# Optimization experiments

Hardware: AMD Instinct MI355X
Metric: run time of the kernel (lower is better)

Reference implementation:

```python
import jax, jax.numpy as jnp
import numpy as np

N_NODES = 100000
IN_DIM = 128
OUT_DIM = 128


def setup_inputs() -> dict:
    key = jax.random.key(0)
    ks = jax.random.split(key, 10)
    # entry counts must be multiples of the edge arity (shape)
    e1, e2, e3 = 300000, 600000, 600000  # arities 1, 2, 3 -> 300k/300k/200k hyperedges
    return {
        "x": jax.random.normal(ks[0], (N_NODES, IN_DIM), dtype=jnp.float32),
        "edge_idx_r1": jax.random.randint(ks[1], (2, e1), 0, N_NODES, dtype=jnp.int32),
        "edge_idx_r2": jax.random.randint(ks[2], (2, e2), 0, N_NODES, dtype=jnp.int32),
        "edge_idx_r3": jax.random.randint(ks[3], (2, e3), 0, N_NODES, dtype=jnp.int32),
        "A_r1": jax.random.normal(ks[4], (IN_DIM * 1, OUT_DIM), dtype=jnp.float32) * np.sqrt(2.0 / (IN_DIM * 1 + OUT_DIM)),
        "A_r2": jax.random.normal(ks[5], (IN_DIM * 2, OUT_DIM), dtype=jnp.float32) * np.sqrt(2.0 / (IN_DIM * 2 + OUT_DIM)),
        "A_r3": jax.random.normal(ks[6], (IN_DIM * 3, OUT_DIM), dtype=jnp.float32) * np.sqrt(2.0 / (IN_DIM * 3 + OUT_DIM)),
        "C_w": jax.random.normal(ks[7], (OUT_DIM, IN_DIM), dtype=jnp.float32) * (1.0 / np.sqrt(IN_DIM)),
        "C_b": jax.random.normal(ks[8], (OUT_DIM,), dtype=jnp.float32) * 0.01,
    }


def _edge_type_messages(x, edge_idx, A, arity, n_nodes):
    # edge_idx: [2, groups*arity]; row0 = src node ids, row1 reshaped -> dest = col 0
    dest = edge_idx[1].reshape(-1, arity)[:, 0]              # [groups]
    src = x[edge_idx[0]].reshape(-1, x.shape[1] * arity)     # [groups, in_dim*arity]
    msg = src @ A                                            # [groups, out_dim]
    # degree normalization within this edge type (== 1/counts from torch.unique)
    counts = jnp.zeros((n_nodes,), dtype=msg.dtype).at[dest].add(1.0)
    msg = msg * (1.0 / counts[dest])[:, None]
    return dest, msg


def reference(x, edge_idx_r1, edge_idx_r2, edge_idx_r3, A_r1, A_r2, A_r3, C_w, C_b):
    n = x.shape[0]
    agg = jnp.zeros((n, C_w.shape[0]), dtype=x.dtype)
    for ei, A, arity in ((edge_idx_r1, A_r1, 1), (edge_idx_r2, A_r2, 2), (edge_idx_r3, A_r3, 3)):
        dest, msg = _edge_type_messages(x, ei, A, arity, n)
        agg = agg.at[dest].add(msg)
    return x @ C_w.T + C_b + agg
```

## Files before the change

### kernel.cpp

```cpp
#include <hip/hip_runtime.h>

#define N_NODES 100000
#define DIM 128

typedef __attribute__((ext_vector_type(8))) short bf16x8;
typedef __attribute__((ext_vector_type(4))) float f32x4;
typedef __attribute__((ext_vector_type(8))) unsigned short ushort8;

__device__ __forceinline__ unsigned short f2bf(float f) {
    union { float f; unsigned u; } v; v.f = f;
    unsigned u = v.u + 0x7FFFu + ((v.u >> 16) & 1u);
    return (unsigned short)(u >> 16);
}
__device__ __forceinline__ float bl(unsigned u) { return __uint_as_float(u << 16); }
__device__ __forceinline__ float bh(unsigned u) { return __uint_as_float(u & 0xFFFF0000u); }

__device__ __forceinline__ void gload_lds16(const void* g, void* l) {
    __builtin_amdgcn_global_load_lds((const __attribute__((address_space(1))) void*)g,
                                     (__attribute__((address_space(3))) void*)l, 16, 0, 0);
}

__device__ __forceinline__ void acc2(float4& a, uint2 v) {
    a.x += bl(v.x); a.y += bh(v.x); a.z += bl(v.y); a.w += bh(v.y);
}
__device__ __forceinline__ void red4(float4& a) {
    a.x += __shfl_xor(a.x, 32); a.y += __shfl_xor(a.y, 32);
    a.z += __shfl_xor(a.z, 32); a.w += __shfl_xor(a.w, 32);
}
__device__ __forceinline__ uint2 pack4s(float4 a, float inv) {
    uint2 r;
    r.x = (unsigned)f2bf(a.x * inv) | ((unsigned)f2bf(a.y * inv) << 16);
    r.y = (unsigned)f2bf(a.z * inv) | ((unsigned)f2bf(a.w * inv) << 16);
    return r;
}

__global__ void prep_kernel(const float* __restrict__ x, unsigned short* __restrict__ xb,
                            int n8, const int* __restrict__ e1d,
                            const int* __restrict__ e2d, const int* __restrict__ e3d,
                            int ng1, int ng12, int ngall, int* __restrict__ counts,
                            const float* __restrict__ A1, const float* __restrict__ A2,
                            const float* __restrict__ A3, const float* __restrict__ Cw,
                            unsigned short* __restrict__ bts, int nxblocks) {
    if ((int)blockIdx.x < nxblocks) {
        int i = blockIdx.x * 256 + threadIdx.x;
        if (i < n8) {
            const float4* p = reinterpret_cast<const float4*>(x) + (size_t)i * 2;
            float4 a = p[0], b = p[1];
            ushort8 o;
            o[0] = f2bf(a.x); o[1] = f2bf(a.y); o[2] = f2bf(a.z); o[3] = f2bf(a.w);
            o[4] = f2bf(b.x); o[5] = f2bf(b.y); o[6] = f2bf(b.z); o[7] = f2bf(b.w);
            *reinterpret_cast<ushort8*>(xb + (size_t)i * 8) = o;
        }
        if (i < ng1) atomicAdd(&counts[e1d[i]], 1);
        else if (i < ng12) atomicAdd(&counts[N_NODES + e2d[(size_t)(i - ng1) * 2]], 1);
        else if (i < ngall) atomicAdd(&counts[2 * N_NODES + e3d[(size_t)(i - ng12) * 3]], 1);
    } else {
        int kg = (blockIdx.x - nxblocks) * 2 + (threadIdx.x >> 7);
        int c = threadIdx.x & 127;
        float v;
        int slice, kp;
        if (kg < 128)      { slice = 0; kp = kg; v = A1[(size_t)kg * 128 + c]; }
        else if (kg < 384) { int k = kg - 128; slice = 1 + (k >> 7); kp = k & 127; v = A2[(size_t)k * 128 + c]; }
        else if (kg < 768) { int k = kg - 384; slice = 3 + (k >> 7); kp = k & 127; v = A3[(size_t)k * 128 + c]; }
        else               { int k = kg - 768; slice = 6; kp = k; v = Cw[(size_t)c * 128 + k]; }
        bts[(size_t)slice * 16384 + c * 128 + kp] = f2bf(v);
    }
}

__global__ __launch_bounds__(256) void scan_p1(const int* __restrict__ counts,
                                               int* __restrict__ partials) {
    __shared__ int red[256];
    int type = blockIdx.y, blk = blockIdx.x, tid = threadIdx.x;
    int base = blk * 4096 + tid * 16;
    int s = 0;
#pragma unroll
    for (int j = 0; j < 16; ++j) {
        int i = base + j;
        s += (i < N_NODES) ? counts[(size_t)type * N_NODES + i] : 0;
    }
    red[tid] = s;
    __syncthreads();
    for (int off = 128; off > 0; off >>= 1) {
        if (tid < off) red[tid] += red[tid + off];
        __syncthreads();
    }
    if (tid == 0) partials[type * 32 + blk] = red[0];
}

__global__ __launch_bounds__(256) void scan_p3(const int* __restrict__ counts,
                                               const int* __restrict__ partials,
                                               int* __restrict__ cursor) {
    __shared__ int tsum[256];
    __shared__ int baseoff;
    int type = blockIdx.y, blk = blockIdx.x, tid = threadIdx.x;
    if (tid == 0) {
        int r = 0;
        for (int b = 0; b < blk; ++b) r += partials[type * 32 + b];
        baseoff = r;
    }
    int base = blk * 4096 + tid * 16;
    int v[16];
    int s = 0;
#pragma unroll
    for (int j = 0; j < 16; ++j) {
        int i = base + j;
        v[j] = (i < N_NODES) ? counts[(size_t)type * N_NODES + i] : 0;
        s += v[j];
    }
    tsum[tid] = s;
    __syncthreads();
    for (int off = 1; off < 256; off <<= 1) {
        int t2 = (tid >= off) ? tsum[tid - off] : 0;
        __syncthreads();
        tsum[tid] += t2;
        __syncthreads();
    }
    int run = tsum[tid] - s + baseoff;
#pragma unroll
    for (int j = 0; j < 16; ++j) {
        int i = base + j;
        if (i < N_NODES) cursor[(size_t)type * N_NODES + i] = run;
        run += v[j];
    }
}

__global__ void scatter_all_kernel(const int* __restrict__ e1, const int* __restrict__ e2,
                                   const int* __restrict__ e3, int ne1, int ne2, int ne3,
                                   int ng1, int ng12, int ngall, int* __restrict__ cursor,
                                   int* __restrict__ s1, int2* __restrict__ s2,
                                   int4* __restrict__ s3) {
    int g = blockIdx.x * 256 + threadIdx.x;
    if (g < ng1) {
        int d = e1[ne1 + g];
        s1[atomicAdd(&cursor[d], 1)] = e1[g] << 8;
    } else if (g < ng12) {
        int k = g - ng1;
        int d = e2[ne2 + 2 * (size_t)k];
        int2 v; v.x = e2[2 * (size_t)k] << 8; v.y = e2[2 * (size_t)k + 1] << 8;
        s2[atomicAdd(&cursor[N_NODES + d], 1)] = v;
    } else if (g < ngall) {
        int k = g - ng12;
        int d = e3[ne3 + 3 * (size_t)k];
        int4 v; v.x = e3[3 * (size_t)k] << 8; v.y = e3[3 * (size_t)k + 1] << 8;
        v.z = e3[3 * (size_t)k + 2] << 8; v.w = 0;
        s3[atomicAdd(&cursor[2 * N_NODES + d], 1)] = v;
    }
}

__global__ __launch_bounds__(256) void aggregate_x_kernel(
    const unsigned short* __restrict__ xb,
    const int* __restrict__ s1, const int2* __restrict__ s2, const int4* __restrict__ s3,
    const int* __restrict__ counts, const int* __restrict__ ends,
    unsigned short* __restrict__ gbf)
{
    int d = blockIdx.x * 4 + (threadIdx.x >> 6);
    if (d >= N_NODES) return;
    const int l = threadIdx.x & 63, hw = l >> 5, sl = l & 31;
    const char* xp = (const char*)xb + sl * 8;
    float4 a0 = {0,0,0,0}, a1 = {0,0,0,0}, a2 = {0,0,0,0};
    float4 a3 = {0,0,0,0}, a4 = {0,0,0,0}, a5 = {0,0,0,0};

    const int c1 = counts[d], c2 = counts[N_NODES + d], c3 = counts[2 * N_NODES + d];
    const int E1 = ends[d], E2 = ends[N_NODES + d], E3 = ends[2 * N_NODES + d];

    {
        int i = E1 - c1 + hw;
        for (; i + 2 < E1; i += 4) {
            int o0 = s1[i], o1 = s1[i + 2];
            uint2 v0 = *reinterpret_cast<const uint2*>(xp + o0);
            uint2 v1 = *reinterpret_cast<const uint2*>(xp + o1);
            acc2(a0, v0); acc2(a0, v1);
        }
        if (i < E1) acc2(a0, *reinterpret_cast<const uint2*>(xp + s1[i]));
    }
    {
        int i = E2 - c2 + hw;
        for (; i + 2 < E2; i += 4) {
            int2 p0 = s2[i], p1 = s2[i + 2];
            uint2 va0 = *reinterpret_cast<const uint2*>(xp + p0.x);
            uint2 vb0 = *reinterpret_cast<const uint2*>(xp + p0.y);
            uint2 va1 = *reinterpret_cast<const uint2*>(xp + p1.x);
            uint2 vb1 = *reinterpret_cast<const uint2*>(xp + p1.y);
            acc2(a1, va0); acc2(a2, vb0); acc2(a1, va1); acc2(a2, vb1);
        }
        if (i < E2) {
            int2 p = s2[i];
            acc2(a1, *reinterpret_cast<const uint2*>(xp + p.x));
            acc2(a2, *reinterpret_cast<const uint2*>(xp + p.y));
        }
    }
    {
        int i = E3 - c3 + hw;
        for (; i + 2 < E3; i += 4) {
            int4 p0 = s3[i], p1 = s3[i + 2];
            uint2 va0 = *reinterpret_cast<const uint2*>(xp + p0.x);
            uint2 vb0 = *reinterpret_cast<const uint2*>(xp + p0.y);
            uint2 vc0 = *reinterpret_cast<const uint2*>(xp + p0.z);
            uint2 va1 = *reinterpret_cast<const uint2*>(xp + p1.x);
            uint2 vb1 = *reinterpret_cast<const uint2*>(xp + p1.y);
            uint2 vc1 = *reinterpret_cast<const uint2*>(xp + p1.z);
            acc2(a3, va0); acc2(a4, vb0); acc2(a5, vc0);
            acc2(a3, va1); acc2(a4, vb1); acc2(a5, vc1);
        }
        if (i < E3) {
            int4 p = s3[i];
            acc2(a3, *reinterpret_cast<const uint2*>(xp + p.x));
            acc2(a4, *reinterpret_cast<const uint2*>(xp + p.y));
            acc2(a5, *reinterpret_cast<const uint2*>(xp + p.z));
        }
    }
    red4(a0); red4(a1); red4(a2); red4(a3); red4(a4); red4(a5);
    if (hw == 0) {
        const float i1 = c1 ? 1.f / (float)c1 : 0.f;
        const float i2 = c2 ? 1.f / (float)c2 : 0.f;
        const float i3 = c3 ? 1.f / (float)c3 : 0.f;
        *reinterpret_cast<uint2*>(gbf + ((size_t)0 * N_NODES + d) * 128 + sl * 4) = pack4s(a0, i1);
        *reinterpret_cast<uint2*>(gbf + ((size_t)1 * N_NODES + d) * 128 + sl * 4) = pack4s(a1, i2);
        *reinterpret_cast<uint2*>(gbf + ((size_t)2 * N_NODES + d) * 128 + sl * 4) = pack4s(a2, i2);
        *reinterpret_cast<uint2*>(gbf + ((size_t)3 * N_NODES + d) * 128 + sl * 4) = pack4s(a3, i3);
        *reinterpret_cast<uint2*>(gbf + ((size_t)4 * N_NODES + d) * 128 + sl * 4) = pack4s(a4, i3);
        *reinterpret_cast<uint2*>(gbf + ((size_t)5 * N_NODES + d) * 128 + sl * 4) = pack4s(a5, i3);
    }
}

__global__ __launch_bounds__(256, 2) void gemm_out_kernel(
    const unsigned short* __restrict__ xb, const unsigned short* __restrict__ gbf,
    const unsigned short* __restrict__ bts, const float* __restrict__ Cb,
    float* __restrict__ out, int nnodes)
{
    __shared__ __align__(16) char smem[65536];

    const int tid = threadIdx.x;
    const int w = tid >> 6, l = tid & 63;
    const int g0 = blockIdx.x * 128;
    const int lrow = l & 15, lk = l >> 4;
    const int wr = (w & 1) * 64, wc = (w >> 1) * 64;

    const int q = (((l & 7) ^ (l >> 3)) << 4);
    const int inner = q & 63;
    const int rpq = ((l >> 3) << 1) + (q >> 6);

    int aoff[4];
#pragma unroll
    for (int mi = 0; mi < 4; ++mi) {
        int r = wr + mi * 16 + lrow;
        int P = r >> 1;
        aoff[mi] = P * 128 + ((((r & 1) << 6) | (lk << 4)) ^ ((P & 7) << 4));
    }

    f32x4 acc[4][4];
#pragma unroll
    for (int mi = 0; mi < 4; ++mi)
#pragma unroll
        for (int ni = 0; ni < 4; ++ni) acc[mi][ni] = (f32x4){0.f, 0.f, 0.f, 0.f};

    auto STAGE = [&](int c, int buf) {
#pragma unroll
        for (int i = 0; i < 2; ++i) {
            int u = w * 2 + i;
            int r = u * 16 + rpq;
            int row = (g0 + r < nnodes) ? g0 + r : 0;
            const char* src = (c < 6)
                ? (const char*)gbf + ((size_t)c * N_NODES + row) * 256
                : (const char*)xb + (size_t)row * 256;
#pragma unroll
            for (int t2 = 0; t2 < 4; ++t2)
                gload_lds16(src + t2 * 64 + inner, smem + buf * 32768 + t2 * 8192 + u * 1024);
        }
    };

    STAGE(0, 0);
    asm volatile("s_waitcnt vmcnt(0)" ::: "memory");
    __builtin_amdgcn_s_barrier();
    asm volatile("" ::: "memory");

    for (int c = 0; c < 7; ++c) {
        if (c + 1 < 7) STAGE(c + 1, (c + 1) & 1);
        const int bb = (c & 1) * 32768;
        bf16x8 bgall[4][4];
#pragma unroll
        for (int ks = 0; ks < 4; ++ks)
#pragma unroll
            for (int ni = 0; ni < 4; ++ni)
                bgall[ks][ni] = *reinterpret_cast<const bf16x8*>(
                    bts + (size_t)c * 16384 + (wc + ni * 16 + lrow) * 128 + ks * 32 + lk * 8);
#pragma unroll
        for (int ks = 0; ks < 4; ++ks) {
            bf16x8 af[4];
#pragma unroll
            for (int mi = 0; mi < 4; ++mi)
                af[mi] = *reinterpret_cast<const bf16x8*>(smem + bb + ks * 8192 + aoff[mi]);
            __builtin_amdgcn_s_setprio(1);
#pragma unroll
            for (int mi = 0; mi < 4; ++mi)
#pragma unroll
                for (int ni = 0; ni < 4; ++ni)
                    acc[mi][ni] = __builtin_amdgcn_mfma_f32_16x16x32_bf16(
                        af[mi], bgall[ks][ni], acc[mi][ni], 0, 0, 0);
            __builtin_amdgcn_s_setprio(0);
        }
        asm volatile("s_waitcnt vmcnt(0)" ::: "memory");
        __builtin_amdgcn_s_barrier();
        asm volatile("" ::: "memory");
    }

    float bv[4];
#pragma unroll
    for (int ni = 0; ni < 4; ++ni) bv[ni] = Cb[wc + ni * 16 + lrow];
#pragma unroll
    for (int mi = 0; mi < 4; ++mi)
#pragma unroll
        for (int reg = 0; reg < 4; ++reg) {
            int g = g0 + wr + mi * 16 + lk * 4 + reg;
            if (g < nnodes) {
#pragma unroll
                for (int ni = 0; ni < 4; ++ni)
                    out[(size_t)g * DIM + wc + ni * 16 + lrow] = acc[mi][ni][reg] + bv[ni];
            }
        }
}

extern "C" void kernel_launch(void* const* d_in, const int* in_sizes, int n_in,
                              void* d_out, int out_size, void* d_ws, size_t ws_size,
                              hipStream_t stream) {
    const float* x  = (const float*)d_in[0];
    const int*   e1 = (const int*)d_in[1];
    const int*   e2 = (const int*)d_in[2];
    const int*   e3 = (const int*)d_in[3];
    const float* A1 = (const float*)d_in[4];
    const float* A2 = (const float*)d_in[5];
    const float* A3 = (const float*)d_in[6];
    const float* Cw = (const float*)d_in[7];
    const float* Cb = (const float*)d_in[8];
    float* out = (float*)d_out;

    const int ne1 = in_sizes[1] / 2, ne2 = in_sizes[2] / 2, ne3 = in_sizes[3] / 2;
    const int ng1 = ne1, ng2 = ne2 / 2, ng3 = ne3 / 3;
    const int N = N_NODES;

    int*  counts  = (int*)d_ws;
    int*  cursor  = counts + 3 * N;
    int4* s3      = (int4*)(cursor + 3 * N);
    int2* s2      = (int2*)(s3 + ng3);
    int*  s1      = (int*)(s2 + ng2);
    int*  partials = s1 + ng1;
    unsigned short* bts = (unsigned short*)(partials + 128);
    unsigned short* xb  = bts + 7 * 16384;
    unsigned short* gbf = xb + (size_t)N * 128;

    const int ngall = ng1 + ng2 + ng3;
    const int n8 = N * DIM / 8;
    const int nxblocks = (n8 + 255) / 256;

    hipMemsetAsync(counts, 0, (size_t)3 * N * sizeof(int), stream);
    prep_kernel<<<nxblocks + 448, 256, 0, stream>>>(
        x, xb, n8, e1 + ne1, e2 + ne2, e3 + ne3, ng1, ng1 + ng2, ngall, counts,
        A1, A2, A3, Cw, bts, nxblocks);
    scan_p1<<<dim3(25, 3), 256, 0, stream>>>(counts, partials);
    scan_p3<<<dim3(25, 3), 256, 0, stream>>>(counts, partials, cursor);
    scatter_all_kernel<<<(ngall + 255) / 256, 256, 0, stream>>>(
        e1, e2, e3, ne1, ne2, ne3, ng1, ng1 + ng2, ngall, cursor, s1, s2, s3);
    aggregate_x_kernel<<<(N + 3) / 4, 256, 0, stream>>>(
        xb, s1, s2, s3, counts, cursor, gbf);
    gemm_out_kernel<<<(N + 127) / 128, 256, 0, stream>>>(xb, gbf, bts, Cb, out, N);
}
```

Measured before the change: 265.8 us.

## Fuse scan and scatter into one cooperative kernel; double-buffer B fragments in GEMM

Replaces the two scan kernels and the scatter kernel with a single cooperative kernel of 1024 blocks that uses grid-wide syncs between the partial-sum, prefix-scan and scatter phases. This removes two kernel launches and the gaps between them, at the cost of two grid barriers and a grid-stride scatter loop over fewer threads. Separately, the output GEMM now prefetches the next chunk's B fragments into registers while the current chunk computes, with the chunk loop fully unrolled. The prefetch raises register pressure and could lower occupancy.

Result: slower. 425.9 us (+60.2%).

```diff
diff --git a/kernel.cpp b/kernel.cpp
--- a/kernel.cpp
+++ b/kernel.cpp
@@ -1,4 +1,7 @@
 #include <hip/hip_runtime.h>
+#include <hip/hip_cooperative_groups.h>
+
+namespace cg = cooperative_groups;
 
 #define N_NODES 100000
 #define DIM 128
@@ -67,83 +70,89 @@
     }
 }
 
-__global__ __launch_bounds__(256) void scan_p1(const int* __restrict__ counts,
-                                               int* __restrict__ partials) {
-    __shared__ int red[256];
-    int type = blockIdx.y, blk = blockIdx.x, tid = threadIdx.x;
-    int base = blk * 4096 + tid * 16;
-    int s = 0;
-#pragma unroll
-    for (int j = 0; j < 16; ++j) {
-        int i = base + j;
-        s += (i < N_NODES) ? counts[(size_t)type * N_NODES + i] : 0;
-    }
-    red[tid] = s;
-    __syncthreads();
-    for (int off = 128; off > 0; off >>= 1) {
-        if (tid < off) red[tid] += red[tid + off];
-        __syncthreads();
-    }
-    if (tid == 0) partials[type * 32 + blk] = red[0];
-}
-
-__global__ __launch_bounds__(256) void scan_p3(const int* __restrict__ counts,
-                                               const int* __restrict__ partials,
-                                               int* __restrict__ cursor) {
+__global__ __launch_bounds__(256) void sort_coop_kernel(
+    const int* __restrict__ e1, const int* __restrict__ e2, const int* __restrict__ e3,
+    int ne1, int ne2, int ne3, int ng1, int ng12, int ngall,
+    const int* __restrict__ counts, int* __restrict__ partials, int* __restrict__ cursor,
+    int* __restrict__ s1, int2* __restrict__ s2, int4* __restrict__ s3)
+{
+    cg::grid_group grid = cg::this_grid();
     __shared__ int tsum[256];
     __shared__ int baseoff;
-    int type = blockIdx.y, blk = blockIdx.x, tid = threadIdx.x;
-    if (tid == 0) {
-        int r = 0;
-        for (int b = 0; b < blk; ++b) r += partials[type * 32 + b];
-        baseoff = r;
-    }
-    int base = blk * 4096 + tid * 16;
-    int v[16];
-    int s = 0;
-#pragma unroll
-    for (int j = 0; j < 16; ++j) {
-        int i = base + j;
-        v[j] = (i < N_NODES) ? counts[(size_t)type * N_NODES + i] : 0;
-        s += v[j];
-    }
-    tsum[tid] = s;
-    __syncthreads();
-    for (int off = 1; off < 256; off <<= 1) {
-        int t2 = (tid >= off) ? tsum[tid - off] : 0;
+    const int tid = threadIdx.x;
+    const int nb = gridDim.x;
+
+    for (int tile = blockIdx.x; tile < 75; tile += nb) {
+        int type = tile / 25, blk = tile % 25;
+        int base = blk * 4096 + tid * 16;
+        int s = 0;
+#pragma unroll
+        for (int j = 0; j < 16; ++j) {
+            int i = base + j;
+            s += (i < N_NODES) ? counts[(size_t)type * N_NODES + i] : 0;
+        }
+        tsum[tid] = s;
         __syncthreads();
-        tsum[tid] += t2;
+        for (int off = 128; off > 0; off >>= 1) {
+            if (tid < off) tsum[tid] += tsum[tid + off];
+            __syncthreads();
+        }
+        if (tid == 0) partials[type * 32 + blk] = tsum[0];
         __syncthreads();
     }
-    int run = tsum[tid] - s + baseoff;
-#pragma unroll
-    for (int j = 0; j < 16; ++j) {
-        int i = base + j;
-        if (i < N_NODES) cursor[(size_t)type * N_NODES + i] = run;
-        run += v[j];
-    }
-}
-
-__global__ void scatter_all_kernel(const int* __restrict__ e1, const int* __restrict__ e2,
-                                   const int* __restrict__ e3, int ne1, int ne2, int ne3,
-                                   int ng1, int ng12, int ngall, int* __restrict__ cursor,
-                                   int* __restrict__ s1, int2* __restrict__ s2,
-                                   int4* __restrict__ s3) {
-    int g = blockIdx.x * 256 + threadIdx.x;
-    if (g < ng1) {
-        int d = e1[ne1 + g];
-        s1[atomicAdd(&cursor[d], 1)] = e1[g] << 8;
-    } else if (g < ng12) {
-        int k = g - ng1;
-        int d = e2[ne2 + 2 * (size_t)k];
-        int2 v; v.x = e2[2 * (size_t)k] << 8; v.y = e2[2 * (size_t)k + 1] << 8;
-        s2[atomicAdd(&cursor[N_NODES + d], 1)] = v;
-    } else if (g < ngall) {
-        int k = g - ng12;
-        int d = e3[ne3 + 3 * (size_t)k];
-        int4 v; v.x = e3[3 * (size_t)k] << 8; v.y = e3[3 * (size_t)k + 1] << 8;
-        v.z = e3[3 * (size_t)k + 2] << 8; v.w = 0;
-        s3[atomicAdd(&cursor[2 * N_NODES + d], 1)] = v;
+    grid.sync();
+
+    for (int tile = blockIdx.x; tile < 75; tile += nb) {
+        int type = tile / 25, blk = tile % 25;
+        if (tid == 0) {
+            int r = 0;
+            for (int b = 0; b < blk; ++b) r += partials[type * 32 + b];
+            baseoff = r;
+        }
+        int base = blk * 4096 + tid * 16;
+        int v[16];
+        int s = 0;
+#pragma unroll
+        for (int j = 0; j < 16; ++j) {
+            int i = base + j;
+            v[j] = (i < N_NODES) ? counts[(size_t)type * N_NODES + i] : 0;
+            s += v[j];
+        }
+        tsum[tid] = s;
+        __syncthreads();
+        for (int off = 1; off < 256; off <<= 1) {
+            int t2 = (tid >= off) ? tsum[tid - off] : 0;
+            __syncthreads();
+            tsum[tid] += t2;
+            __syncthreads();
+        }
+        int run = tsum[tid] - s + baseoff;
+#pragma unroll
+        for (int j = 0; j < 16; ++j) {
+            int i = base + j;
+            if (i < N_NODES) cursor[(size_t)type * N_NODES + i] = run;
+            run += v[j];
+        }
+        __syncthreads();
+    }
+    grid.sync();
+
+    for (int g = blockIdx.x * 256 + tid; g < ngall; g += nb * 256) {
+        if (g < ng1) {
+            int d = e1[ne1 + g];
+            s1[atomicAdd(&cursor[d], 1)] = e1[g] << 8;
+        } else if (g < ng12) {
+            int k = g - ng1;
+            int d = e2[ne2 + 2 * (size_t)k];
+            int2 v; v.x = e2[2 * (size_t)k] << 8; v.y = e2[2 * (size_t)k + 1] << 8;
+            s2[atomicAdd(&cursor[N_NODES + d], 1)] = v;
+        } else {
+            int k = g - ng12;
+            int d = e3[ne3 + 3 * (size_t)k];
+            int4 v; v.x = e3[3 * (size_t)k] << 8; v.y = e3[3 * (size_t)k + 1] << 8;
+            v.z = e3[3 * (size_t)k + 2] << 8; v.w = 0;
+            s3[atomicAdd(&cursor[2 * N_NODES + d], 1)] = v;
+        }
     }
 }
 
@@ -269,21 +278,28 @@
         }
     };
 
+    auto LOADB = [&](int c, bf16x8 (&dst)[4][4]) {
+#pragma unroll
+        for (int ks = 0; ks < 4; ++ks)
+#pragma unroll
+            for (int ni = 0; ni < 4; ++ni)
+                dst[ks][ni] = *reinterpret_cast<const bf16x8*>(
+                    bts + (size_t)c * 16384 + (wc + ni * 16 + lrow) * 128 + ks * 32 + lk * 8);
+    };
+
+    bf16x8 bgA[4][4], bgB[4][4];
     STAGE(0, 0);
+    LOADB(0, bgA);
     asm volatile("s_waitcnt vmcnt(0)" ::: "memory");
     __builtin_amdgcn_s_barrier();
     asm volatile("" ::: "memory");
 
-    for (int c = 0; c < 7; ++c) {
-        if (c + 1 < 7) STAGE(c + 1, (c + 1) & 1);
+    auto BODY = [&](int c, bf16x8 (&cur)[4][4], bf16x8 (&nxt)[4][4]) {
+        if (c + 1 < 7) {
+            STAGE(c + 1, (c + 1) & 1);
+            LOADB(c + 1, nxt);
+        }
         const int bb = (c & 1) * 32768;
-        bf16x8 bgall[4][4];
-#pragma unroll
-        for (int ks = 0; ks < 4; ++ks)
-#pragma unroll
-            for (int ni = 0; ni < 4; ++ni)
-                bgall[ks][ni] = *reinterpret_cast<const bf16x8*>(
-                    bts + (size_t)c * 16384 + (wc + ni * 16 + lrow) * 128 + ks * 32 + lk * 8);
 #pragma unroll
         for (int ks = 0; ks < 4; ++ks) {
             bf16x8 af[4];
@@ -296,13 +312,21 @@
 #pragma unroll
                 for (int ni = 0; ni < 4; ++ni)
                     acc[mi][ni] = __builtin_amdgcn_mfma_f32_16x16x32_bf16(
-                        af[mi], bgall[ks][ni], acc[mi][ni], 0, 0, 0);
+                        af[mi], cur[ks][ni], acc[mi][ni], 0, 0, 0);
             __builtin_amdgcn_s_setprio(0);
         }
         asm volatile("s_waitcnt vmcnt(0)" ::: "memory");
         __builtin_amdgcn_s_barrier();
         asm volatile("" ::: "memory");
-    }
+    };
+
+    BODY(0, bgA, bgB);
+    BODY(1, bgB, bgA);
+    BODY(2, bgA, bgB);
+    BODY(3, bgB, bgA);
+    BODY(4, bgA, bgB);
+    BODY(5, bgB, bgA);
+    BODY(6, bgA, bgB);
 
     float bv[4];
 #pragma unroll
@@ -334,8 +358,8 @@
     const float* Cb = (const float*)d_in[8];
     float* out = (float*)d_out;
 
-    const int ne1 = in_sizes[1] / 2, ne2 = in_sizes[2] / 2, ne3 = in_sizes[3] / 2;
-    const int ng1 = ne1, ng2 = ne2 / 2, ng3 = ne3 / 3;
+    int ne1 = in_sizes[1] / 2, ne2 = in_sizes[2] / 2, ne3 = in_sizes[3] / 2;
+    int ng1 = ne1, ng2 = ne2 / 2, ng3 = ne3 / 3;
     const int N = N_NODES;
 
     int*  counts  = (int*)d_ws;
@@ -348,18 +372,26 @@
     unsigned short* xb  = bts + 7 * 16384;
     unsigned short* gbf = xb + (size_t)N * 128;
 
-    const int ngall = ng1 + ng2 + ng3;
+    int ngall = ng1 + ng2 + ng3;
+    int ng12 = ng1 + ng2;
     const int n8 = N * DIM / 8;
     const int nxblocks = (n8 + 255) / 256;
 
     hipMemsetAsync(counts, 0, (size_t)3 * N * sizeof(int), stream);
     prep_kernel<<<nxblocks + 448, 256, 0, stream>>>(
-        x, xb, n8, e1 + ne1, e2 + ne2, e3 + ne3, ng1, ng1 + ng2, ngall, counts,
+        x, xb, n8, e1 + ne1, e2 + ne2, e3 + ne3, ng1, ng12, ngall, counts,
         A1, A2, A3, Cw, bts, nxblocks);
-    scan_p1<<<dim3(25, 3), 256, 0, stream>>>(counts, partials);
-    scan_p3<<<dim3(25, 3), 256, 0, stream>>>(counts, partials, cursor);
-    scatter_all_kernel<<<(ngall + 255) / 256, 256, 0, stream>>>(
-        e1, e2, e3, ne1, ne2, ne3, ng1, ng1 + ng2, ngall, cursor, s1, s2, s3);
+
+    {
+        const int* e1a = e1; const int* e2a = e2; const int* e3a = e3;
+        int* countsa = counts; int* partialsa = partials; int* cursora = cursor;
+        int* s1a = s1; int2* s2a = s2; int4* s3a = s3;
+        void* args[] = {&e1a, &e2a, &e3a, &ne1, &ne2, &ne3, &ng1, &ng12, &ngall,
+                        &countsa, &partialsa, &cursora, &s1a, &s2a, &s3a};
+        hipLaunchCooperativeKernel((void*)sort_coop_kernel, dim3(1024), dim3(256),
+                                   args, 0, stream);
+    }
+
     aggregate_x_kernel<<<(N + 3) / 4, 256, 0, stream>>>(
         xb, s1, s2, s3, counts, cursor, gbf);
     gemm_out_kernel<<<(N + 127) / 128, 256, 0, stream>>>(xb, gbf, bts, Cb, out, N);
```

## Restructure output GEMM into fine-grained 4-buffer K-step pipeline with smaller LDS

Applied to the files above, without the earlier changes.

The output GEMM kernel used to stage a whole 128-wide K chunk into double-buffered 64KB LDS and wait for it fully before computing. It now splits the work into 28 K-steps of 32, each with an 8KB LDS slice in a 4-slot ring. Loads run three steps ahead, B fragments two steps ahead, and partial vmcnt waits replace the full drains. LDS use drops to 32KB and launch bounds rise to 3 blocks per CU, aiming for more occupancy and latency overlap. The cost is twice as many barriers per step and higher register pressure, which may cause spills under the tighter launch bound.

Measured after the change: 253.1 us. 1.05x faster.

```diff
diff --git a/kernel.cpp b/kernel.cpp
--- a/kernel.cpp
+++ b/kernel.cpp
@@ -223,12 +223,12 @@
     }
 }
 
-__global__ __launch_bounds__(256, 2) void gemm_out_kernel(
+__global__ __launch_bounds__(256, 3) void gemm_out_kernel(
     const unsigned short* __restrict__ xb, const unsigned short* __restrict__ gbf,
     const unsigned short* __restrict__ bts, const float* __restrict__ Cb,
     float* __restrict__ out, int nnodes)
 {
-    __shared__ __align__(16) char smem[65536];
+    __shared__ __align__(16) char smem[32768];
 
     const int tid = threadIdx.x;
     const int w = tid >> 6, l = tid & 63;
@@ -248,61 +248,75 @@
         aoff[mi] = P * 128 + ((((r & 1) << 6) | (lk << 4)) ^ ((P & 7) << 4));
     }
 
+    const char* srow[2];
+#pragma unroll
+    for (int i = 0; i < 2; ++i) {
+        int u = w * 2 + i;
+        int r = u * 16 + rpq;
+        int row = (g0 + r < nnodes) ? g0 + r : 0;
+        srow[i] = (const char*)(size_t)row;
+    }
+    const int u0 = w * 2, r0 = u0 * 16 + rpq, r1 = (u0 + 1) * 16 + rpq;
+    const int row0 = (g0 + r0 < nnodes) ? g0 + r0 : 0;
+    const int row1 = (g0 + r1 < nnodes) ? g0 + r1 : 0;
+
     f32x4 acc[4][4];
 #pragma unroll
     for (int mi = 0; mi < 4; ++mi)
 #pragma unroll
         for (int ni = 0; ni < 4; ++ni) acc[mi][ni] = (f32x4){0.f, 0.f, 0.f, 0.f};
 
-    auto STAGE = [&](int c, int buf) {
-#pragma unroll
-        for (int i = 0; i < 2; ++i) {
-            int u = w * 2 + i;
-            int r = u * 16 + rpq;
-            int row = (g0 + r < nnodes) ? g0 + r : 0;
-            const char* src = (c < 6)
-                ? (const char*)gbf + ((size_t)c * N_NODES + row) * 256
-                : (const char*)xb + (size_t)row * 256;
-#pragma unroll
-            for (int t2 = 0; t2 < 4; ++t2)
-                gload_lds16(src + t2 * 64 + inner, smem + buf * 32768 + t2 * 8192 + u * 1024);
-        }
+    auto STAGE = [&](int s) {
+        const int c = s >> 2, ks = s & 3;
+        const int buf = s & 3;
+        const char* b0 = (c < 6) ? (const char*)gbf + ((size_t)c * N_NODES + row0) * 256
+                                 : (const char*)xb + (size_t)row0 * 256;
+        const char* b1 = (c < 6) ? (const char*)gbf + ((size_t)c * N_NODES + row1) * 256
+                                 : (const char*)xb + (size_t)row1 * 256;
+        gload_lds16(b0 + ks * 64 + inner, smem + buf * 8192 + u0 * 1024);
+        gload_lds16(b1 + ks * 64 + inner, smem + buf * 8192 + (u0 + 1) * 1024);
     };
 
-    STAGE(0, 0);
-    asm volatile("s_waitcnt vmcnt(0)" ::: "memory");
-    __builtin_amdgcn_s_barrier();
-    asm volatile("" ::: "memory");
-
-    for (int c = 0; c < 7; ++c) {
-        if (c + 1 < 7) STAGE(c + 1, (c + 1) & 1);
-        const int bb = (c & 1) * 32768;
-        bf16x8 bgall[4][4];
-#pragma unroll
-        for (int ks = 0; ks < 4; ++ks)
-#pragma unroll
-            for (int ni = 0; ni < 4; ++ni)
-                bgall[ks][ni] = *reinterpret_cast<const bf16x8*>(
-                    bts + (size_t)c * 16384 + (wc + ni * 16 + lrow) * 128 + ks * 32 + lk * 8);
-#pragma unroll
-        for (int ks = 0; ks < 4; ++ks) {
-            bf16x8 af[4];
-#pragma unroll
-            for (int mi = 0; mi < 4; ++mi)
-                af[mi] = *reinterpret_cast<const bf16x8*>(smem + bb + ks * 8192 + aoff[mi]);
-            __builtin_amdgcn_s_setprio(1);
-#pragma unroll
-            for (int mi = 0; mi < 4; ++mi)
-#pragma unroll
-                for (int ni = 0; ni < 4; ++ni)
-                    acc[mi][ni] = __builtin_amdgcn_mfma_f32_16x16x32_bf16(
-                        af[mi], bgall[ks][ni], acc[mi][ni], 0, 0, 0);
-            __builtin_amdgcn_s_setprio(0);
-        }
-        asm volatile("s_waitcnt vmcnt(0)" ::: "memory");
-        __builtin_amdgcn_s_barrier();
-        asm volatile("" ::: "memory");
-    }
+    auto LOADB = [&](int s, bf16x8 (&dst)[4]) {
+        const int c = s >> 2, ks = s & 3;
+#pragma unroll
+        for (int ni = 0; ni < 4; ++ni)
+            dst[ni] = *reinterpret_cast<const bf16x8*>(
+                bts + (size_t)c * 16384 + (wc + ni * 16 + lrow) * 128 + ks * 32 + lk * 8);
+    };
+
+    bf16x8 bg[3][4];
+    STAGE(0); STAGE(1); STAGE(2);
+    LOADB(0, bg[0]); LOADB(1, bg[1]);
+
+#define KEEPV(S) (4 * ((27 - (S)) < 0 ? 0 : ((27 - (S)) < 2 ? (27 - (S)) : 2)) + \
+                  2 * ((26 - (S)) < 0 ? 0 : ((26 - (S)) < 2 ? (26 - (S)) : 2)))
+
+#define GBODY(S)                                                                   \
+    {                                                                              \
+        if ((S) + 3 < 28) STAGE((S) + 3);                                          \
+        if ((S) + 2 < 28) LOADB((S) + 2, bg[((S) + 2) % 3]);                       \
+        asm volatile("s_waitcnt vmcnt(%0)" ::"i"(KEEPV(S)) : "memory");            \
+        __builtin_amdgcn_s_barrier();                                              \
+        asm volatile("" ::: "memory");                                             \
+        bf16x8 af[4];                                                              \
+        _Pragma("unroll") for (int mi = 0; mi < 4; ++mi) af[mi] =                  \
+            *reinterpret_cast<const bf16x8*>(smem + ((S) & 3) * 8192 + aoff[mi]);  \
+        __builtin_amdgcn_s_setprio(1);                                             \
+        _Pragma("unroll") for (int mi = 0; mi < 4; ++mi)                           \
+            _Pragma("unroll") for (int ni = 0; ni < 4; ++ni) acc[mi][ni] =         \
+                __builtin_amdgcn_mfma_f32_16x16x32_bf16(af[mi], bg[(S) % 3][ni],   \
+                                                        acc[mi][ni], 0, 0, 0);     \
+        __builtin_amdgcn_s_setprio(0);                                             \
+        __builtin_amdgcn_s_barrier();                                              \
+    }
+
+    GBODY(0)  GBODY(1)  GBODY(2)  GBODY(3)  GBODY(4)  GBODY(5)  GBODY(6)
+    GBODY(7)  GBODY(8)  GBODY(9)  GBODY(10) GBODY(11) GBODY(12) GBODY(13)
+    GBODY(14) GBODY(15) GBODY(16) GBODY(17) GBODY(18) GBODY(19) GBODY(20)
+    GBODY(21) GBODY(22) GBODY(23) GBODY(24) GBODY(25) GBODY(26) GBODY(27)
+#undef GBODY
+#undef KEEPV
 
     float bv[4];
 #pragma unroll
@@ -349,17 +363,18 @@
     unsigned short* gbf = xb + (size_t)N * 128;
 
     const int ngall = ng1 + ng2 + ng3;
+    const int ng12 = ng1 + ng2;
     const int n8 = N * DIM / 8;
     const int nxblocks = (n8 + 255) / 256;
 
     hipMemsetAsync(counts, 0, (size_t)3 * N * sizeof(int), stream);
     prep_kernel<<<nxblocks + 448, 256, 0, stream>>>(
-        x, xb, n8, e1 + ne1, e2 + ne2, e3 + ne3, ng1, ng1 + ng2, ngall, counts,
+        x, xb, n8, e1 + ne1, e2 + ne2, e3 + ne3, ng1, ng12, ngall, counts,
         A1, A2, A3, Cw, bts, nxblocks);
     scan_p1<<<dim3(25, 3), 256, 0, stream>>>(counts, partials);
     scan_p3<<<dim3(25, 3), 256, 0, stream>>>(counts, partials, cursor);
     scatter_all_kernel<<<(ngall + 255) / 256, 256, 0, stream>>>(
-        e1, e2, e3, ne1, ne2, ne3, ng1, ng1 + ng2, ngall, cursor, s1, s2, s3);
+        e1, e2, e3, ne1, ne2, ne3, ng1, ng12, ngall, cursor, s1, s2, s3);
     aggregate_x_kernel<<<(N + 3) / 4, 256, 0, stream>>>(
         xb, s1, s2, s3, counts, cursor, gbf);
     gemm_out_kernel<<<(N + 127) / 128, 256, 0, stream>>>(xb, gbf, bts, Cb, out, N);
```
